# Optimization experiments

Hardware: AMD Instinct MI355X
Metric: run time of the kernel (lower is better)

## Reference

```python
import jax, jax.numpy as jnp
import numpy as np

TARGET_KAPPA = 1.0 / 61.0
EPS = 1e-10

# --- antisymmetric expansion: 35 independent components (i<j<k) -> (7,7,7) ---
_combos = np.array([(i, j, k) for i in range(7) for j in range(i + 1, 7) for k in range(j + 1, 7)])  # (35,3)
_perm_specs = [((0, 1, 2), 1.0), ((0, 2, 1), -1.0), ((1, 0, 2), -1.0), ((1, 2, 0), 1.0), ((2, 0, 1), 1.0), ((2, 1, 0), -1.0)]
_I = jnp.array(np.concatenate([_combos[:, p[0]] for p, _ in _perm_specs]))
_J = jnp.array(np.concatenate([_combos[:, p[1]] for p, _ in _perm_specs]))
_K = jnp.array(np.concatenate([_combos[:, p[2]] for p, _ in _perm_specs]))
_S = jnp.array(np.concatenate([np.full(35, s, dtype=np.float32) for _, s in _perm_specs]))


def expand_to_antisymmetric(v35):
    # v35: (35,) -> antisymmetric (7,7,7)
    vals = jnp.tile(v35, 6) * _S.astype(v35.dtype)
    return jnp.zeros((7, 7, 7), v35.dtype).at[_I, _J, _K].set(vals)


def _phi_single(xi, W1, b1, W2, b2):
    # xi: (7,) -> antisymmetric 3-form (7,7,7)
    h = jnp.tanh(xi @ W1 + b1)          # (H,)
    v35 = h @ W2 + b2                    # (35,)
    return expand_to_antisymmetric(v35)


def setup_inputs() -> dict:
    key = jax.random.key(0)
    k1, k2, k3 = jax.random.split(key, 3)
    B, H = 32768, 512
    x = jax.random.normal(k1, (B, 7), dtype=jnp.float32)
    W1 = jax.random.normal(k2, (7, H), dtype=jnp.float32) * 0.3
    b1 = jnp.zeros((H,), dtype=jnp.float32)
    W2 = jax.random.normal(k3, (H, 35), dtype=jnp.float32) * 0.05
    b2 = jnp.zeros((35,), dtype=jnp.float32)
    return {"x": x, "W1": W1, "b1": b1, "W2": W2, "b2": b2}


def reference(x, W1, b1, W2, b2):
    f = lambda xi: _phi_single(xi, W1, b1, W2, b2)
    # Jacobian replaces the 35 looped autograd.grad calls: (B,7,7,7,7), last axis = d/dx_l
    jac = jax.vmap(jax.jacfwd(f))(x)
    d_phi = jnp.moveaxis(jac, -1, 1)  # (B, 7(deriv), 7, 7, 7), matching torch layout
    torsion_sq = jnp.sum(d_phi ** 2, axis=(1, 2, 3, 4))  # (B,)
    torsion_norm = jnp.sqrt(torsion_sq + EPS)
    loss = jnp.mean((torsion_norm - TARGET_KAPPA) ** 2)
    return loss, jnp.mean(torsion_norm)
```

## Files before the change

### kernel.cpp

```cpp
#include <hip/hip_runtime.h>
#include <hip/hip_bf16.h>
#include <math.h>

typedef __attribute__((ext_vector_type(8)))  short bf16x8;
typedef __attribute__((ext_vector_type(16))) float f32x16;
typedef unsigned int u32;

#define KAPPA (1.0f/61.0f)
#define NBLK 512
#define SWAP23(r) (((r) & 19) | (((r) & 4) << 1) | (((r) & 8) >> 1))

__device__ __forceinline__ unsigned short f2bf(float f) {
    u32 x = __float_as_uint(f);
    x += 0x7fffu + ((x >> 16) & 1u);
    return (unsigned short)(x >> 16);
}
__device__ __forceinline__ float fast_rcp(float v) {
#if __has_builtin(__builtin_amdgcn_rcpf)
    return __builtin_amdgcn_rcpf(v);
#else
    return 1.0f / v;
#endif
}
__device__ __forceinline__ float exp2_fast(float v) {
#if __has_builtin(__builtin_amdgcn_exp2f)
    return __builtin_amdgcn_exp2f(v);
#else
    return exp2f(v);
#endif
}
__device__ __forceinline__ u32 pack_bf16(float lo, float hi) {
    __hip_bfloat162 p = __float22bfloat162_rn(make_float2(lo, hi));
    return *reinterpret_cast<u32*>(&p);
}

__global__ void build_v(const float* __restrict__ W1, const float* __restrict__ W2,
                        const float* __restrict__ b1,
                        bf16x8* __restrict__ V, bf16x8* __restrict__ Wt) {
    int t = blockIdx.x * blockDim.x + threadIdx.x;
    if (t < 16384) {
        int lane = t & 63, ptile = (t >> 6) & 7, kkg = t >> 9;
        int p  = ptile * 32 + (lane & 31);
        int hb = kkg * 16 + (lane >> 5) * 8;
        bool valid = (p < 245);
        int l7 = valid ? p / 35 : 0;
        int c  = valid ? p - l7 * 35 : 0;
        bf16x8 v;
#pragma unroll
        for (int i = 0; i < 8; ++i) {
            int h = hb + i;
            v[i] = valid ? (short)f2bf(4.0f * W1[l7 * 512 + h] * W2[h * 35 + c]) : (short)0;
        }
        V[t] = v;
    } else if (t < 16384 + 1024) {
        int f = t - 16384;
        int lane = f & 63, htile = f >> 6;
        int row = lane & 31;
        int h = htile * 32 + SWAP23(row);
        bf16x8 v;
#pragma unroll
        for (int i = 0; i < 8; ++i) v[i] = 0;
        if (lane < 32) {
#pragma unroll
            for (int l = 0; l < 7; ++l) v[l] = (short)f2bf(W1[l * 512 + h]);
            v[7] = (short)f2bf(b1[h]);
        }
        Wt[f] = v;
    }
}

__global__ __launch_bounds__(256, 3)
void torsion_main(const float* __restrict__ x,
                  const bf16x8* __restrict__ V, const bf16x8* __restrict__ Wt,
                  float* __restrict__ partials) {
    __shared__ __align__(16) u32 Gb[2][8][64 * 4];
    __shared__ float red[4][2][32];

    const int tid  = threadIdx.x;
    const int lane = tid & 63;
    const int w    = tid >> 6;
    const int blk  = blockIdx.x;
    const int rt   = w & 1;
    const int ht   = w >> 1;

    bf16x8 xf;
#pragma unroll
    for (int i = 0; i < 8; ++i) xf[i] = 0;
    if (lane < 32) {
        const float* xp = x + ((size_t)blk * 64 + rt * 32 + lane) * 7;
#pragma unroll
        for (int l = 0; l < 7; ++l) xf[l] = (short)f2bf(xp[l]);
        xf[7] = (short)f2bf(1.0f);
    }

    f32x16 acc[2][2];
#pragma unroll
    for (int pt = 0; pt < 2; ++pt)
#pragma unroll
        for (int r2 = 0; r2 < 2; ++r2)
#pragma unroll
            for (int e = 0; e < 16; ++e) acc[pt][r2][e] = 0.0f;

    auto pre_pack = [&](bf16x8 wf, u32 d[8]) {
        f32x16 p;
#pragma unroll
        for (int e = 0; e < 16; ++e) p[e] = 0.0f;
        p = __builtin_amdgcn_mfma_f32_32x32x16_bf16(wf, xf, p, 0, 0, 0);
#pragma unroll
        for (int j = 0; j < 8; ++j) {
            float t0 = exp2_fast(-2.8853901f * fabsf(p[2 * j]));
            float r0 = fast_rcp(1.0f + t0);
            float g0 = t0 * r0 * r0;
            float t1 = exp2_fast(-2.8853901f * fabsf(p[2 * j + 1]));
            float r1 = fast_rcp(1.0f + t1);
            float g1 = t1 * r1 * r1;
            d[j] = pack_bf16(g0, g1);
        }
    };
    auto store_g = [&](int buf, const u32 d[8]) {
        *reinterpret_cast<uint4*>(&Gb[buf][(2 * ht + 0) * 2 + rt][lane * 4]) =
            make_uint4(d[0], d[1], d[2], d[3]);
        *reinterpret_cast<uint4*>(&Gb[buf][(2 * ht + 1) * 2 + rt][lane * 4]) =
            make_uint4(d[4], d[5], d[6], d[7]);
    };

    bf16x8 wfn;
    {
        bf16x8 wf0 = Wt[(0 * 2 + ht) * 64 + lane];
        wfn = Wt[(1 * 2 + ht) * 64 + lane];
        u32 d0[8];
        pre_pack(wf0, d0);
        store_g(0, d0);
    }
    __syncthreads();

    for (int c = 0; c < 8; ++c) {
        const int buf = c & 1;

        bf16x8 vreg[8];
#pragma unroll
        for (int ks = 0; ks < 4; ++ks) {
            const int fb = ((c * 4 + ks) * 8 + 2 * w) * 64 + lane;
            vreg[2 * ks]     = V[fb];
            vreg[2 * ks + 1] = V[fb + 64];
        }
        bf16x8 wf2;
        if (c < 6) wf2 = Wt[((c + 2) * 2 + ht) * 64 + lane];

        u32 dn[8];
        if (c < 7) pre_pack(wfn, dn);

        __builtin_amdgcn_s_setprio(1);
#pragma unroll
        for (int ks = 0; ks < 4; ++ks) {
            bf16x8 g0 = *reinterpret_cast<const bf16x8*>(&Gb[buf][ks * 2 + 0][lane * 4]);
            bf16x8 g1 = *reinterpret_cast<const bf16x8*>(&Gb[buf][ks * 2 + 1][lane * 4]);
            acc[0][0] = __builtin_amdgcn_mfma_f32_32x32x16_bf16(vreg[2 * ks],     g0, acc[0][0], 0, 0, 0);
            acc[0][1] = __builtin_amdgcn_mfma_f32_32x32x16_bf16(vreg[2 * ks],     g1, acc[0][1], 0, 0, 0);
            acc[1][0] = __builtin_amdgcn_mfma_f32_32x32x16_bf16(vreg[2 * ks + 1], g0, acc[1][0], 0, 0, 0);
            acc[1][1] = __builtin_amdgcn_mfma_f32_32x32x16_bf16(vreg[2 * ks + 1], g1, acc[1][1], 0, 0, 0);
        }
        __builtin_amdgcn_s_setprio(0);

        if (c < 7) store_g(buf ^ 1, dn);
        wfn = wf2;
        __syncthreads();
    }

#pragma unroll
    for (int r2 = 0; r2 < 2; ++r2) {
        float s = 0.0f;
#pragma unroll
        for (int pt = 0; pt < 2; ++pt)
#pragma unroll
            for (int e = 0; e < 16; ++e) s += acc[pt][r2][e] * acc[pt][r2][e];
        s += __shfl_xor(s, 32);
        if (lane < 32) red[w][r2][lane] = s;
    }
    __syncthreads();

    if (tid < 64) {
        const int li = tid & 31, rr = tid >> 5;
        float q = 6.0f * (red[0][rr][li] + red[1][rr][li] + red[2][rr][li] + red[3][rr][li]);
        float n = sqrtf(q + 1e-10f);
        float d = n - KAPPA;
        float a = d * d, b = n;
#pragma unroll
        for (int m = 1; m <= 32; m <<= 1) {
            a += __shfl_xor(a, m);
            b += __shfl_xor(b, m);
        }
        if (tid == 0) {
            partials[blk]        = a;
            partials[NBLK + blk] = b;
        }
    }
}

__global__ void finalize_k(const float* __restrict__ partials, float* __restrict__ out) {
    __shared__ float sl[256], sn[256];
    int tid = threadIdx.x;
    sl[tid] = partials[tid] + partials[tid + 256];
    sn[tid] = partials[NBLK + tid] + partials[NBLK + tid + 256];
    __syncthreads();
    for (int st = 128; st > 0; st >>= 1) {
        if (tid < st) { sl[tid] += sl[tid + st]; sn[tid] += sn[tid + st]; }
        __syncthreads();
    }
    if (tid == 0) {
        out[0] = sl[0] / 32768.0f;
        out[1] = sn[0] / 32768.0f;
    }
}

extern "C" void kernel_launch(void* const* d_in, const int* in_sizes, int n_in,
                              void* d_out, int out_size, void* d_ws, size_t ws_size,
                              hipStream_t stream) {
    const float* x  = (const float*)d_in[0];
    const float* W1 = (const float*)d_in[1];
    const float* b1 = (const float*)d_in[2];
    const float* W2 = (const float*)d_in[3];

    bf16x8* V        = (bf16x8*)d_ws;
    bf16x8* Wt       = V + 16384;
    float*  partials = (float*)(Wt + 1024);

    build_v<<<68, 256, 0, stream>>>(W1, W2, b1, V, Wt);
    torsion_main<<<NBLK, 256, 0, stream>>>(x, V, Wt, partials);
    finalize_k<<<1, 256, 0, stream>>>(partials, (float*)d_out);
}
```

Before: 24.61 us.

## Double chunk size per barrier in torsion main loop, halving syncthreads count

```diff
diff --git a/kernel.cpp b/kernel.cpp
--- a/kernel.cpp
+++ b/kernel.cpp
@@ -69,11 +69,11 @@
     }
 }
 
-__global__ __launch_bounds__(256, 3)
+__global__ __launch_bounds__(256, 2)
 void torsion_main(const float* __restrict__ x,
                   const bf16x8* __restrict__ V, const bf16x8* __restrict__ Wt,
                   float* __restrict__ partials) {
-    __shared__ __align__(16) u32 Gb[2][8][64 * 4];
+    __shared__ __align__(16) u32 Gb[2][16][64 * 4];
     __shared__ float red[4][2][32];
 
     const int tid  = threadIdx.x;
@@ -117,53 +117,86 @@
             d[j] = pack_bf16(g0, g1);
         }
     };
-    auto store_g = [&](int buf, const u32 d[8]) {
+    auto store_g2 = [&](int buf, const u32 dA[8], const u32 dB[8]) {
         *reinterpret_cast<uint4*>(&Gb[buf][(2 * ht + 0) * 2 + rt][lane * 4]) =
-            make_uint4(d[0], d[1], d[2], d[3]);
+            make_uint4(dA[0], dA[1], dA[2], dA[3]);
         *reinterpret_cast<uint4*>(&Gb[buf][(2 * ht + 1) * 2 + rt][lane * 4]) =
-            make_uint4(d[4], d[5], d[6], d[7]);
+            make_uint4(dA[4], dA[5], dA[6], dA[7]);
+        *reinterpret_cast<uint4*>(&Gb[buf][(2 * (ht + 2) + 0) * 2 + rt][lane * 4]) =
+            make_uint4(dB[0], dB[1], dB[2], dB[3]);
+        *reinterpret_cast<uint4*>(&Gb[buf][(2 * (ht + 2) + 1) * 2 + rt][lane * 4]) =
+            make_uint4(dB[4], dB[5], dB[6], dB[7]);
     };
 
-    bf16x8 wfn;
+    bf16x8 wfnA, wfnB;
     {
-        bf16x8 wf0 = Wt[(0 * 2 + ht) * 64 + lane];
-        wfn = Wt[(1 * 2 + ht) * 64 + lane];
-        u32 d0[8];
-        pre_pack(wf0, d0);
-        store_g(0, d0);
+        bf16x8 wfA = Wt[(0 * 4 + ht) * 64 + lane];
+        bf16x8 wfB = Wt[(0 * 4 + ht + 2) * 64 + lane];
+        wfnA = Wt[(1 * 4 + ht) * 64 + lane];
+        wfnB = Wt[(1 * 4 + ht + 2) * 64 + lane];
+        u32 dA[8], dB[8];
+        pre_pack(wfA, dA);
+        pre_pack(wfB, dB);
+        store_g2(0, dA, dB);
     }
     __syncthreads();
 
-    for (int c = 0; c < 8; ++c) {
+    for (int c = 0; c < 4; ++c) {
         const int buf = c & 1;
 
-        bf16x8 vreg[8];
-#pragma unroll
-        for (int ks = 0; ks < 4; ++ks) {
-            const int fb = ((c * 4 + ks) * 8 + 2 * w) * 64 + lane;
-            vreg[2 * ks]     = V[fb];
-            vreg[2 * ks + 1] = V[fb + 64];
-        }
-        bf16x8 wf2;
-        if (c < 6) wf2 = Wt[((c + 2) * 2 + ht) * 64 + lane];
-
-        u32 dn[8];
-        if (c < 7) pre_pack(wfn, dn);
+        bf16x8 vregA[8];
+#pragma unroll
+        for (int ks = 0; ks < 4; ++ks) {
+            const int fb = ((c * 8 + ks) * 8 + 2 * w) * 64 + lane;
+            vregA[2 * ks]     = V[fb];
+            vregA[2 * ks + 1] = V[fb + 64];
+        }
+        bf16x8 wf2A, wf2B;
+        if (c < 2) {
+            wf2A = Wt[((c + 2) * 4 + ht) * 64 + lane];
+            wf2B = Wt[((c + 2) * 4 + ht + 2) * 64 + lane];
+        }
+
+        u32 dA[8], dB[8];
+        if (c < 3) pre_pack(wfnA, dA);
 
         __builtin_amdgcn_s_setprio(1);
 #pragma unroll
         for (int ks = 0; ks < 4; ++ks) {
             bf16x8 g0 = *reinterpret_cast<const bf16x8*>(&Gb[buf][ks * 2 + 0][lane * 4]);
             bf16x8 g1 = *reinterpret_cast<const bf16x8*>(&Gb[buf][ks * 2 + 1][lane * 4]);
-            acc[0][0] = __builtin_amdgcn_mfma_f32_32x32x16_bf16(vreg[2 * ks],     g0, acc[0][0], 0, 0, 0);
-            acc[0][1] = __builtin_amdgcn_mfma_f32_32x32x16_bf16(vreg[2 * ks],     g1, acc[0][1], 0, 0, 0);
-            acc[1][0] = __builtin_amdgcn_mfma_f32_32x32x16_bf16(vreg[2 * ks + 1], g0, acc[1][0], 0, 0, 0);
-            acc[1][1] = __builtin_amdgcn_mfma_f32_32x32x16_bf16(vreg[2 * ks + 1], g1, acc[1][1], 0, 0, 0);
+            acc[0][0] = __builtin_amdgcn_mfma_f32_32x32x16_bf16(vregA[2 * ks],     g0, acc[0][0], 0, 0, 0);
+            acc[0][1] = __builtin_amdgcn_mfma_f32_32x32x16_bf16(vregA[2 * ks],     g1, acc[0][1], 0, 0, 0);
+            acc[1][0] = __builtin_amdgcn_mfma_f32_32x32x16_bf16(vregA[2 * ks + 1], g0, acc[1][0], 0, 0, 0);
+            acc[1][1] = __builtin_amdgcn_mfma_f32_32x32x16_bf16(vregA[2 * ks + 1], g1, acc[1][1], 0, 0, 0);
         }
         __builtin_amdgcn_s_setprio(0);
 
-        if (c < 7) store_g(buf ^ 1, dn);
-        wfn = wf2;
+        bf16x8 vregB[8];
+#pragma unroll
+        for (int ks = 0; ks < 4; ++ks) {
+            const int fb = ((c * 8 + 4 + ks) * 8 + 2 * w) * 64 + lane;
+            vregB[2 * ks]     = V[fb];
+            vregB[2 * ks + 1] = V[fb + 64];
+        }
+
+        if (c < 3) pre_pack(wfnB, dB);
+
+        __builtin_amdgcn_s_setprio(1);
+#pragma unroll
+        for (int ks = 0; ks < 4; ++ks) {
+            bf16x8 g0 = *reinterpret_cast<const bf16x8*>(&Gb[buf][(4 + ks) * 2 + 0][lane * 4]);
+            bf16x8 g1 = *reinterpret_cast<const bf16x8*>(&Gb[buf][(4 + ks) * 2 + 1][lane * 4]);
+            acc[0][0] = __builtin_amdgcn_mfma_f32_32x32x16_bf16(vregB[2 * ks],     g0, acc[0][0], 0, 0, 0);
+            acc[0][1] = __builtin_amdgcn_mfma_f32_32x32x16_bf16(vregB[2 * ks],     g1, acc[0][1], 0, 0, 0);
+            acc[1][0] = __builtin_amdgcn_mfma_f32_32x32x16_bf16(vregB[2 * ks + 1], g0, acc[1][0], 0, 0, 0);
+            acc[1][1] = __builtin_amdgcn_mfma_f32_32x32x16_bf16(vregB[2 * ks + 1], g1, acc[1][1], 0, 0, 0);
+        }
+        __builtin_amdgcn_s_setprio(0);
+
+        if (c < 3) store_g2(buf ^ 1, dA, dB);
+        wfnA = wf2A;
+        wfnB = wf2B;
         __syncthreads();
     }
 
```

Measured after the change: 24.83 us. About the same (+0.9%).

## Halve rows per block to 32, doubling grid and occupancy, split V loads

Applied to the files above, without the earlier changes.

```diff
diff --git a/kernel.cpp b/kernel.cpp
--- a/kernel.cpp
+++ b/kernel.cpp
@@ -7,7 +7,7 @@
 typedef unsigned int u32;
 
 #define KAPPA (1.0f/61.0f)
-#define NBLK 512
+#define NBLK 1024
 #define SWAP23(r) (((r) & 19) | (((r) & 4) << 1) | (((r) & 8) >> 1))
 
 __device__ __forceinline__ unsigned short f2bf(float f) {
@@ -69,37 +69,33 @@
     }
 }
 
-__global__ __launch_bounds__(256, 3)
+__global__ __launch_bounds__(256, 4)
 void torsion_main(const float* __restrict__ x,
                   const bf16x8* __restrict__ V, const bf16x8* __restrict__ Wt,
                   float* __restrict__ partials) {
     __shared__ __align__(16) u32 Gb[2][8][64 * 4];
-    __shared__ float red[4][2][32];
+    __shared__ float red[4][32];
 
     const int tid  = threadIdx.x;
     const int lane = tid & 63;
     const int w    = tid >> 6;
     const int blk  = blockIdx.x;
-    const int rt   = w & 1;
-    const int ht   = w >> 1;
 
     bf16x8 xf;
 #pragma unroll
     for (int i = 0; i < 8; ++i) xf[i] = 0;
     if (lane < 32) {
-        const float* xp = x + ((size_t)blk * 64 + rt * 32 + lane) * 7;
+        const float* xp = x + ((size_t)blk * 32 + lane) * 7;
 #pragma unroll
         for (int l = 0; l < 7; ++l) xf[l] = (short)f2bf(xp[l]);
         xf[7] = (short)f2bf(1.0f);
     }
 
-    f32x16 acc[2][2];
+    f32x16 acc[2];
 #pragma unroll
     for (int pt = 0; pt < 2; ++pt)
 #pragma unroll
-        for (int r2 = 0; r2 < 2; ++r2)
-#pragma unroll
-            for (int e = 0; e < 16; ++e) acc[pt][r2][e] = 0.0f;
+        for (int e = 0; e < 16; ++e) acc[pt][e] = 0.0f;
 
     auto pre_pack = [&](bf16x8 wf, u32 d[8]) {
         f32x16 p;
@@ -118,75 +114,88 @@
         }
     };
     auto store_g = [&](int buf, const u32 d[8]) {
-        *reinterpret_cast<uint4*>(&Gb[buf][(2 * ht + 0) * 2 + rt][lane * 4]) =
+        *reinterpret_cast<uint4*>(&Gb[buf][2 * w + 0][lane * 4]) =
             make_uint4(d[0], d[1], d[2], d[3]);
-        *reinterpret_cast<uint4*>(&Gb[buf][(2 * ht + 1) * 2 + rt][lane * 4]) =
+        *reinterpret_cast<uint4*>(&Gb[buf][2 * w + 1][lane * 4]) =
             make_uint4(d[4], d[5], d[6], d[7]);
     };
 
     bf16x8 wfn;
     {
-        bf16x8 wf0 = Wt[(0 * 2 + ht) * 64 + lane];
-        wfn = Wt[(1 * 2 + ht) * 64 + lane];
+        bf16x8 wf0 = Wt[(0 * 4 + w) * 64 + lane];
+        wfn = Wt[(1 * 4 + w) * 64 + lane];
         u32 d0[8];
         pre_pack(wf0, d0);
         store_g(0, d0);
     }
     __syncthreads();
 
-    for (int c = 0; c < 8; ++c) {
+#pragma unroll
+    for (int c = 0; c < 4; ++c) {
         const int buf = c & 1;
 
-        bf16x8 vreg[8];
-#pragma unroll
-        for (int ks = 0; ks < 4; ++ks) {
-            const int fb = ((c * 4 + ks) * 8 + 2 * w) * 64 + lane;
-            vreg[2 * ks]     = V[fb];
-            vreg[2 * ks + 1] = V[fb + 64];
+        bf16x8 vregA[8];
+#pragma unroll
+        for (int ks = 0; ks < 4; ++ks) {
+            const int fb = ((c * 8 + ks) * 8 + 2 * w) * 64 + lane;
+            vregA[2 * ks]     = V[fb];
+            vregA[2 * ks + 1] = V[fb + 64];
         }
         bf16x8 wf2;
-        if (c < 6) wf2 = Wt[((c + 2) * 2 + ht) * 64 + lane];
+        if (c < 2) wf2 = Wt[((c + 2) * 4 + w) * 64 + lane];
 
         u32 dn[8];
-        if (c < 7) pre_pack(wfn, dn);
+        if (c < 3) pre_pack(wfn, dn);
 
         __builtin_amdgcn_s_setprio(1);
 #pragma unroll
         for (int ks = 0; ks < 4; ++ks) {
-            bf16x8 g0 = *reinterpret_cast<const bf16x8*>(&Gb[buf][ks * 2 + 0][lane * 4]);
-            bf16x8 g1 = *reinterpret_cast<const bf16x8*>(&Gb[buf][ks * 2 + 1][lane * 4]);
-            acc[0][0] = __builtin_amdgcn_mfma_f32_32x32x16_bf16(vreg[2 * ks],     g0, acc[0][0], 0, 0, 0);
-            acc[0][1] = __builtin_amdgcn_mfma_f32_32x32x16_bf16(vreg[2 * ks],     g1, acc[0][1], 0, 0, 0);
-            acc[1][0] = __builtin_amdgcn_mfma_f32_32x32x16_bf16(vreg[2 * ks + 1], g0, acc[1][0], 0, 0, 0);
-            acc[1][1] = __builtin_amdgcn_mfma_f32_32x32x16_bf16(vreg[2 * ks + 1], g1, acc[1][1], 0, 0, 0);
+            bf16x8 g = *reinterpret_cast<const bf16x8*>(&Gb[buf][ks][lane * 4]);
+            acc[0] = __builtin_amdgcn_mfma_f32_32x32x16_bf16(vregA[2 * ks],     g, acc[0], 0, 0, 0);
+            acc[1] = __builtin_amdgcn_mfma_f32_32x32x16_bf16(vregA[2 * ks + 1], g, acc[1], 0, 0, 0);
         }
         __builtin_amdgcn_s_setprio(0);
 
-        if (c < 7) store_g(buf ^ 1, dn);
+        bf16x8 vregB[8];
+#pragma unroll
+        for (int ks = 0; ks < 4; ++ks) {
+            const int fb = ((c * 8 + 4 + ks) * 8 + 2 * w) * 64 + lane;
+            vregB[2 * ks]     = V[fb];
+            vregB[2 * ks + 1] = V[fb + 64];
+        }
+
+        __builtin_amdgcn_s_setprio(1);
+#pragma unroll
+        for (int ks = 0; ks < 4; ++ks) {
+            bf16x8 g = *reinterpret_cast<const bf16x8*>(&Gb[buf][4 + ks][lane * 4]);
+            acc[0] = __builtin_amdgcn_mfma_f32_32x32x16_bf16(vregB[2 * ks],     g, acc[0], 0, 0, 0);
+            acc[1] = __builtin_amdgcn_mfma_f32_32x32x16_bf16(vregB[2 * ks + 1], g, acc[1], 0, 0, 0);
+        }
+        __builtin_amdgcn_s_setprio(0);
+
+        if (c < 3) store_g(buf ^ 1, dn);
         wfn = wf2;
         __syncthreads();
     }
 
-#pragma unroll
-    for (int r2 = 0; r2 < 2; ++r2) {
+    {
         float s = 0.0f;
 #pragma unroll
         for (int pt = 0; pt < 2; ++pt)
 #pragma unroll
-            for (int e = 0; e < 16; ++e) s += acc[pt][r2][e] * acc[pt][r2][e];
+            for (int e = 0; e < 16; ++e) s += acc[pt][e] * acc[pt][e];
         s += __shfl_xor(s, 32);
-        if (lane < 32) red[w][r2][lane] = s;
+        if (lane < 32) red[w][lane] = s;
     }
     __syncthreads();
 
-    if (tid < 64) {
-        const int li = tid & 31, rr = tid >> 5;
-        float q = 6.0f * (red[0][rr][li] + red[1][rr][li] + red[2][rr][li] + red[3][rr][li]);
+    if (tid < 32) {
+        float q = 6.0f * (red[0][tid] + red[1][tid] + red[2][tid] + red[3][tid]);
         float n = sqrtf(q + 1e-10f);
         float d = n - KAPPA;
         float a = d * d, b = n;
 #pragma unroll
-        for (int m = 1; m <= 32; m <<= 1) {
+        for (int m = 1; m <= 16; m <<= 1) {
             a += __shfl_xor(a, m);
             b += __shfl_xor(b, m);
         }
@@ -200,8 +209,9 @@
 __global__ void finalize_k(const float* __restrict__ partials, float* __restrict__ out) {
     __shared__ float sl[256], sn[256];
     int tid = threadIdx.x;
-    sl[tid] = partials[tid] + partials[tid + 256];
-    sn[tid] = partials[NBLK + tid] + partials[NBLK + tid + 256];
+    sl[tid] = partials[tid] + partials[tid + 256] + partials[tid + 512] + partials[tid + 768];
+    sn[tid] = partials[NBLK + tid] + partials[NBLK + tid + 256]
+            + partials[NBLK + tid + 512] + partials[NBLK + tid + 768];
     __syncthreads();
     for (int st = 128; st > 0; st >>= 1) {
         if (tid < st) { sl[tid] += sl[tid + st]; sn[tid] += sn[tid + st]; }
```

Result: slower. 26.83 us (+9.0%).
